# Optimization experiments

Measured on AMD Instinct MI355X. Metric: run time of the kernel, lower is better.

Reference implementation:

```python
import jax, jax.numpy as jnp
import numpy as np
from functools import partial

F_DIM, DETER, STOCH, HEADS = 1024, 256, 1024, 8
HD = F_DIM // HEADS  # 128
LN_EPS = 1e-5


def _layer_norm(x, g, b):
    m = jnp.mean(x, axis=-1, keepdims=True)
    v = jnp.var(x, axis=-1, keepdims=True)
    return (x - m) * jax.lax.rsqrt(v + LN_EPS) * g + b


def _forward(emb_vision, emb_text, emb_proprio, noise, h0, s0,
             proj_vision_w, proj_vision_b, proj_text_w, proj_text_b,
             proj_proprio_w, proj_proprio_b,
             attn_in_w, attn_in_b, attn_out_w, attn_out_b, importance,
             fuse_w1, fuse_b1, fuse_w2, fuse_b2, ln_g, ln_b,
             gru_w_ih, gru_w_hh, gru_b_ih, gru_b_hh,
             prior_w, prior_b, post_w, post_b):
    B, T = emb_vision.shape[:2]
    N = B * T
    # --- multimodal fusion, vectorized over all (B,T) steps ---
    pv = emb_vision @ proj_vision_w.T + proj_vision_b      # (B,T,F)
    pt = emb_text @ proj_text_w.T + proj_text_b
    pp = emb_proprio @ proj_proprio_w.T + proj_proprio_b
    stacked = jnp.stack([pv, pt, pp], axis=2).reshape(N, 3, F_DIM)  # (N,3,F)
    # self-attention over the 3 modality tokens (nn.MultiheadAttention)
    qkv = stacked @ attn_in_w.T + attn_in_b                 # (N,3,3F)
    q, k, v = jnp.split(qkv, 3, axis=-1)
    q = q.reshape(N, 3, HEADS, HD)
    k = k.reshape(N, 3, HEADS, HD)
    v = v.reshape(N, 3, HEADS, HD)
    scores = jnp.einsum('nqhd,nkhd->nhqk', q, k) / jnp.sqrt(jnp.float32(HD))
    attn = jax.nn.softmax(scores, axis=-1)
    att = jnp.einsum('nhqk,nkhd->nqhd', attn, v).reshape(N, 3, F_DIM)
    att = att @ attn_out_w.T + attn_out_b
    imp = jax.nn.softmax(importance)
    weighted = att * imp[None, :, None]
    concat = weighted.reshape(N, 3 * F_DIM)
    fused = jax.nn.relu(concat @ fuse_w1.T + fuse_b1) @ fuse_w2.T + fuse_b2
    fused = _layer_norm(fused, ln_g, ln_b).reshape(B, T, F_DIM)

    # --- sequential RSSM rollout ---
    def step(carry, xt):
        h, s = carry
        f_t, n_t = xt
        x = jnp.concatenate([s, f_t], axis=-1)              # (B, 2048)
        gi = x @ gru_w_ih.T + gru_b_ih                      # (B, 3*DETER)
        gh = h @ gru_w_hh.T + gru_b_hh
        ir, iz, inn = jnp.split(gi, 3, axis=-1)
        hr, hz, hn = jnp.split(gh, 3, axis=-1)
        r = jax.nn.sigmoid(ir + hr)
        z = jax.nn.sigmoid(iz + hz)
        n = jnp.tanh(inn + r * hn)
        h_new = (1.0 - z) * n + z * h
        prior = h_new @ prior_w.T + prior_b                 # (B, STOCH)
        post = jnp.concatenate([h_new, f_t], -1) @ post_w.T + post_b
        s_new = post + n_t                                  # reparameterized sample (unit std)
        out = jnp.concatenate([h_new, s_new, prior, post], axis=-1)
        return (h_new, s_new), out

    fused_T = jnp.swapaxes(fused, 0, 1)                     # (T,B,F)
    noise_T = jnp.swapaxes(noise, 0, 1)
    _, outs = jax.lax.scan(step, (h0, s0), (fused_T, noise_T))
    return jnp.swapaxes(outs, 0, 1)                         # (B,T,256+1024+1024+1024)


def setup_inputs() -> dict:
    key = jax.random.key(0)
    ks = iter(jax.random.split(key, 40))
    B, T = 64, 128

    def w(shape):
        fan_in = shape[-1]
        return jax.random.normal(next(ks), shape, jnp.float32) / np.sqrt(fan_in)

    d = {
        'emb_vision': jax.random.normal(next(ks), (B, T, 512), jnp.float32),
        'emb_text': jax.random.normal(next(ks), (B, T, 512), jnp.float32),
        'emb_proprio': jax.random.normal(next(ks), (B, T, 256), jnp.float32),
        'noise': jax.random.normal(next(ks), (B, T, STOCH), jnp.float32),
        'h0': jnp.zeros((B, DETER), jnp.float32),
        's0': jnp.zeros((B, STOCH), jnp.float32),
        'proj_vision_w': w((F_DIM, 512)), 'proj_vision_b': jnp.zeros((F_DIM,), jnp.float32),
        'proj_text_w': w((F_DIM, 512)), 'proj_text_b': jnp.zeros((F_DIM,), jnp.float32),
        'proj_proprio_w': w((F_DIM, 256)), 'proj_proprio_b': jnp.zeros((F_DIM,), jnp.float32),
        'attn_in_w': w((3 * F_DIM, F_DIM)), 'attn_in_b': jnp.zeros((3 * F_DIM,), jnp.float32),
        'attn_out_w': w((F_DIM, F_DIM)), 'attn_out_b': jnp.zeros((F_DIM,), jnp.float32),
        'importance': jnp.ones((3,), jnp.float32),
        'fuse_w1': w((F_DIM, 3 * F_DIM)), 'fuse_b1': jnp.zeros((F_DIM,), jnp.float32),
        'fuse_w2': w((F_DIM, F_DIM)), 'fuse_b2': jnp.zeros((F_DIM,), jnp.float32),
        'ln_g': jnp.ones((F_DIM,), jnp.float32), 'ln_b': jnp.zeros((F_DIM,), jnp.float32),
        'gru_w_ih': w((3 * DETER, F_DIM + STOCH)), 'gru_w_hh': w((3 * DETER, DETER)),
        'gru_b_ih': jnp.zeros((3 * DETER,), jnp.float32), 'gru_b_hh': jnp.zeros((3 * DETER,), jnp.float32),
        'prior_w': w((STOCH, DETER)), 'prior_b': jnp.zeros((STOCH,), jnp.float32),
        'post_w': w((STOCH, DETER + F_DIM)), 'post_b': jnp.zeros((STOCH,), jnp.float32),
    }
    return d


def reference(emb_vision, emb_text, emb_proprio, noise, h0, s0,
              proj_vision_w, proj_vision_b, proj_text_w, proj_text_b,
              proj_proprio_w, proj_proprio_b,
              attn_in_w, attn_in_b, attn_out_w, attn_out_b, importance,
              fuse_w1, fuse_b1, fuse_w2, fuse_b2, ln_g, ln_b,
              gru_w_ih, gru_w_hh, gru_b_ih, gru_b_hh,
              prior_w, prior_b, post_w, post_b):
    return _forward(emb_vision, emb_text, emb_proprio, noise, h0, s0,
                    proj_vision_w, proj_vision_b, proj_text_w, proj_text_b,
                    proj_proprio_w, proj_proprio_b,
                    attn_in_w, attn_in_b, attn_out_w, attn_out_b, importance,
                    fuse_w1, fuse_b1, fuse_w2, fuse_b2, ln_g, ln_b,
                    gru_w_ih, gru_w_hh, gru_b_ih, gru_b_hh,
                    prior_w, prior_b, post_w, post_b)
```

## Files before the change

kernel.cpp:

```cpp
#include <hip/hip_runtime.h>
#include <cstdint>
#include <cstddef>

#define F4(p)  (*(reinterpret_cast<float4*>(p)))
#define CF4(p) (*(reinterpret_cast<const float4*>(p)))

typedef __attribute__((ext_vector_type(8))) short short8;
typedef __attribute__((ext_vector_type(4))) float f32x4;
typedef __attribute__((ext_vector_type(4))) int i32x4;

__device__ __forceinline__ float bf2f(unsigned short h) {
  return __uint_as_float(((unsigned int)h) << 16);
}
__device__ __forceinline__ unsigned short f2bf(float x) {
  unsigned int u = __float_as_uint(x);
  return (unsigned short)((u + 0x7FFFu + ((u >> 16) & 1u)) >> 16);
}

#if __has_builtin(__builtin_amdgcn_global_load_lds)
#define USE_GLL 1
#else
#define USE_GLL 0
#endif
#if __has_builtin(__builtin_amdgcn_sched_barrier)
#define SCHED_BARRIER() __builtin_amdgcn_sched_barrier(0)
#else
#define SCHED_BARRIER()
#endif

__device__ __forceinline__ void stage16(unsigned short* lds_lane,
                                        unsigned short* lds_wavebase,
                                        const unsigned short* g) {
#if USE_GLL
  __builtin_amdgcn_global_load_lds(
      (const __attribute__((address_space(1))) unsigned int*)g,
      (__attribute__((address_space(3))) unsigned int*)lds_wavebase, 16, 0, 0);
#else
  *(short8*)lds_lane = *(const short8*)g;
#endif
}

__device__ __forceinline__ i32x4 coh_load16(const void* p) {
  i32x4 r;
  asm volatile("global_load_dwordx4 %0, %1, off sc0"
               : "=v"(r) : "v"(p) : "memory");
  return r;
}
__device__ __forceinline__ void coh_store16(void* p, i32x4 v) {
  asm volatile("global_store_dwordx4 %0, %1, off sc0"
               :: "v"(p), "v"(v) : "memory");
}

__device__ __forceinline__ float fsigmoid(float x) {
  return 1.0f / (1.0f + __expf(-x));
}
__device__ __forceinline__ float ftanh(float x) {
  float ax = fabsf(x);
  float e = __expf(2.0f * ax);
  float t = 1.0f - 2.0f / (e + 1.0f);
  return copysignf(t, x);
}

__global__ __launch_bounds__(256) void gemm_bf(
    const unsigned short* __restrict__ A, int lda,
    const unsigned short* __restrict__ A2, int lda2, int kSplit,
    const unsigned short* __restrict__ B, int ldb,
    const unsigned short* __restrict__ B2, int ldb2, int nSplit,
    void* __restrict__ Cv, int ldc, int K,
    const float* __restrict__ bias,
    const float* __restrict__ src, int ldsrc, int src_c0,
    const float* __restrict__ scale_ptr, int relu, int obf16, int qperm)
{
  __shared__ unsigned short As[128 * 64];
  __shared__ unsigned short Bs[128 * 64];
  const int tid = threadIdx.x;
  const int wv = tid >> 6, ln = tid & 63;
  const int wm = wv >> 1, wn = wv & 1;
  const size_t gm0 = (size_t)blockIdx.y * 128;
  const size_t gn0 = (size_t)blockIdx.x * 128;

  f32x4 acc[4][4];
  #pragma unroll
  for (int i = 0; i < 4; ++i)
    #pragma unroll
    for (int j = 0; j < 4; ++j) acc[i][j] = (f32x4){0.f, 0.f, 0.f, 0.f};

  for (int kk = 0; kk < K; kk += 64) {
    const unsigned short* Ause = A; int lduse = lda; int kkA = kk;
    if (A2 != nullptr && kk >= kSplit) { Ause = A2; lduse = lda2; kkA = kk - kSplit; }
    #pragma unroll
    for (int j = 0; j < 4; ++j) {
      int idx = j * 256 + tid;
      int r = idx >> 3, u = idx & 7;
      int ksw = (u ^ (r & 7)) << 3;
      const unsigned short* ga = Ause + (gm0 + r) * lduse + kkA + ksw;
      stage16(&As[idx * 8], &As[(idx & ~63) * 8], ga);
      size_t nr = gn0 + r;
      const unsigned short* gb = (nr < (size_t)nSplit)
          ? B + nr * ldb + kk + ksw
          : B2 + (nr - nSplit) * ldb2 + kk + ksw;
      stage16(&Bs[idx * 8], &Bs[(idx & ~63) * 8], gb);
    }
    __syncthreads();
    #pragma unroll
    for (int ks = 0; ks < 2; ++ks) {
      short8 af[4], bfv[4];
      #pragma unroll
      for (int mi = 0; mi < 4; ++mi) {
        int r = wm * 64 + mi * 16 + (ln & 15);
        int u = (ks * 4 + (ln >> 4)) ^ (r & 7);
        af[mi] = *(const short8*)&As[(r * 8 + u) * 8];
      }
      #pragma unroll
      for (int nj = 0; nj < 4; ++nj) {
        int r = wn * 64 + nj * 16 + (ln & 15);
        int u = (ks * 4 + (ln >> 4)) ^ (r & 7);
        bfv[nj] = *(const short8*)&Bs[(r * 8 + u) * 8];
      }
      #pragma unroll
      for (int mi = 0; mi < 4; ++mi)
        #pragma unroll
        for (int nj = 0; nj < 4; ++nj)
          acc[mi][nj] = __builtin_amdgcn_mfma_f32_16x16x32_bf16(
              af[mi], bfv[nj], acc[mi][nj], 0, 0, 0);
    }
    __syncthreads();
  }

  float sc = scale_ptr ? *scale_ptr : 1.0f;
  #pragma unroll
  for (int nj = 0; nj < 4; ++nj) {
    int gc = (int)gn0 + wn * 64 + nj * 16 + (ln & 15);
    float bv = bias ? bias[gc] : 0.f;
    #pragma unroll
    for (int mi = 0; mi < 4; ++mi) {
      #pragma unroll
      for (int qq = 0; qq < 4; ++qq) {
        int gr = (int)gm0 + wm * 64 + mi * 16 + ((ln >> 4) << 2) + qq;
        float v = acc[mi][nj][qq] * sc + bv;
        if (src && gc >= src_c0) v += src[(size_t)gr * ldsrc + (gc - src_c0)];
        if (relu) v = fmaxf(v, 0.f);
        if (qperm) {
          int t = gr & 127, bq = gr >> 7;
          int g = gc >> 8, d = gc & 255;
          int ddq = d >> 5, doff = d & 31;
          int wq = bq >> 4;
          int lq = (bq & 15) + ((doff >> 3) << 4);
          size_t qi = (((((size_t)t * 8 + ddq) * 3 + g) * 4 + wq) * 64 + lq) * 8
                      + (doff & 7);
          ((float*)Cv)[qi] = v;
        } else if (obf16) {
          ((unsigned short*)Cv)[(size_t)gr * ldc + gc] = f2bf(v);
        } else {
          ((float*)Cv)[(size_t)gr * ldc + gc] = v;
        }
      }
    }
  }
}

__global__ __launch_bounds__(256) void cvt_bf(
    const float* __restrict__ in, unsigned short* __restrict__ outp, int n4)
{
  int i = blockIdx.x * 256 + threadIdx.x;
  if (i < n4) {
    float4 v = CF4(in + (size_t)i * 4);
    ushort4 o;
    o.x = f2bf(v.x); o.y = f2bf(v.y); o.z = f2bf(v.z); o.w = f2bf(v.w);
    *(ushort4*)(outp + (size_t)i * 4) = o;
  }
}

__global__ __launch_bounds__(256) void transpose_bf(
    const float* __restrict__ in, int ldin, unsigned short* __restrict__ outp, int R)
{
  __shared__ float tile[32][33];
  int c0 = blockIdx.x * 32, r0 = blockIdx.y * 32;
  int tx = threadIdx.x & 31, ty = threadIdx.x >> 5;
  #pragma unroll
  for (int i = ty; i < 32; i += 8)
    tile[i][tx] = in[(size_t)(r0 + i) * ldin + c0 + tx];
  __syncthreads();
  #pragma unroll
  for (int i = ty; i < 32; i += 8)
    outp[(size_t)(c0 + i) * R + r0 + tx] = f2bf(tile[tx][i]);
}

__global__ __launch_bounds__(64) void matvec3(
    const float* __restrict__ A,
    const float* __restrict__ x0, const float* __restrict__ x1,
    const float* __restrict__ x2, const float* __restrict__ aib,
    float* __restrict__ outp)
{
  int i = blockIdx.x, t = threadIdx.x;
  const float* Ar = A + (size_t)i * 1024;
  float s0 = 0.f, s1 = 0.f, s2 = 0.f;
  for (int k = t * 4; k < 1024; k += 256) {
    float4 a = CF4(Ar + k);
    float4 v0 = CF4(x0 + k), v1 = CF4(x1 + k), v2 = CF4(x2 + k);
    s0 += a.x*v0.x + a.y*v0.y + a.z*v0.z + a.w*v0.w;
    s1 += a.x*v1.x + a.y*v1.y + a.z*v1.z + a.w*v1.w;
    s2 += a.x*v2.x + a.y*v2.y + a.z*v2.z + a.w*v2.w;
  }
  #pragma unroll
  for (int m = 32; m > 0; m >>= 1) {
    s0 += __shfl_xor(s0, m); s1 += __shfl_xor(s1, m); s2 += __shfl_xor(s2, m);
  }
  if (t == 0) {
    float b = aib[i];
    outp[i] = s0 + b; outp[3072 + i] = s1 + b; outp[6144 + i] = s2 + b;
  }
}

__global__ __launch_bounds__(64) void matvec_nt(
    const float* __restrict__ A, int lda,
    const float* __restrict__ x, const float* __restrict__ badd,
    float* __restrict__ outp, int K)
{
  int i = blockIdx.x, t = threadIdx.x;
  const float* Ar = A + (size_t)i * lda;
  float s = 0.f;
  for (int k = t * 4; k < K; k += 256) {
    float4 a = CF4(Ar + k);
    float4 xx = CF4(x + k);
    s += a.x*xx.x + a.y*xx.y + a.z*xx.z + a.w*xx.w;
  }
  #pragma unroll
  for (int m = 32; m > 0; m >>= 1) s += __shfl_xor(s, m);
  if (t == 0) outp[i] = s + (badd ? badd[i] : 0.f);
}

__global__ __launch_bounds__(256) void imp_rep_k(
    const float* __restrict__ importance, const float* __restrict__ aob,
    float* __restrict__ imp, float* __restrict__ rep)
{
  __shared__ float si[3];
  if (threadIdx.x == 0) {
    float a = importance[0], b = importance[1], c = importance[2];
    float mx = fmaxf(a, fmaxf(b, c));
    float ea = expf(a - mx), eb = expf(b - mx), ec = expf(c - mx);
    float inv = 1.f / (ea + eb + ec);
    si[0] = ea * inv; si[1] = eb * inv; si[2] = ec * inv;
    imp[0] = si[0]; imp[1] = si[1]; imp[2] = si[2];
  }
  __syncthreads();
  for (int idx = threadIdx.x; idx < 3072; idx += 256)
    rep[idx] = si[idx >> 10] * aob[idx & 1023];
}

__global__ __launch_bounds__(256) void bias_prep(
    const float* __restrict__ gbih, const float* __restrict__ gbhh,
    const float* __restrict__ prb, float* __restrict__ cb768,
    float* __restrict__ cb2048)
{
  int i = blockIdx.x * 256 + threadIdx.x;
  if (i < 768) cb768[i] = gbih[i] + (i < 512 ? gbhh[i] : 0.f);
  if (i < 2048) cb2048[i] = (i < 1024) ? prb[i] : 0.f;
}

__global__ __launch_bounds__(256) void attn3(
    const unsigned short* __restrict__ qkv, unsigned short* __restrict__ att)
{
  const int n = blockIdx.x;
  const unsigned short* row = qkv + (size_t)n * 9216;
  __shared__ float qk[6144];
  __shared__ float sc[72];
  __shared__ float pw[72];
  const int t = threadIdx.x;
  for (int idx = t; idx < 768; idx += 256) {
    int m = idx >> 7;
    int off = (idx & 127) << 3;
    const unsigned short* srcp = (m < 3) ? (row + m * 3072 + off)
                                         : (row + (m - 3) * 3072 + 1024 + off);
    short8 v = *(const short8*)srcp;
    float* dst = &qk[m * 1024 + off];
    #pragma unroll
    for (int j = 0; j < 8; ++j) dst[j] = bf2f(((const unsigned short*)&v)[j]);
  }
  __syncthreads();
  if (t < 72) {
    int h = t / 9, i = (t % 9) / 3, j = t % 3;
    const float* qp = &qk[i * 1024 + h * 128];
    const float* kp = &qk[3072 + j * 1024 + h * 128];
    float s = 0.f;
    int rot = (t & 31) * 4;
    for (int d2 = 0; d2 < 128; ++d2) {
      int dx = (d2 + rot) & 127;
      s += qp[dx] * kp[dx];
    }
    sc[t] = s * 0.08838834764831845f;
  }
  __syncthreads();
  if (t < 24) {
    int base = t * 3;
    float a = sc[base], b = sc[base + 1], c = sc[base + 2];
    float mx = fmaxf(a, fmaxf(b, c));
    float ea = expf(a - mx), eb = expf(b - mx), ec = expf(c - mx);
    float inv = 1.f / (ea + eb + ec);
    pw[base] = ea * inv; pw[base + 1] = eb * inv; pw[base + 2] = ec * inv;
  }
  __syncthreads();
  unsigned short* outp = att + (size_t)n * 3072;
  #pragma unroll
  for (int rep = 0; rep < 3; ++rep) {
    int idx = (rep * 256 + t) << 2;
    int i = idx >> 10;
    int hd = idx & 1023;
    int h = hd >> 7;
    int pb = (h * 3 + i) * 3;
    float w0 = pw[pb], w1 = pw[pb + 1], w2 = pw[pb + 2];
    ushort4 v0 = *(const ushort4*)(row + 2048 + hd);
    ushort4 v1 = *(const ushort4*)(row + 3072 + 2048 + hd);
    ushort4 v2 = *(const ushort4*)(row + 6144 + 2048 + hd);
    ushort4 o;
    o.x = f2bf(w0 * bf2f(v0.x) + w1 * bf2f(v1.x) + w2 * bf2f(v2.x));
    o.y = f2bf(w0 * bf2f(v0.y) + w1 * bf2f(v1.y) + w2 * bf2f(v2.y));
    o.z = f2bf(w0 * bf2f(v0.z) + w1 * bf2f(v1.z) + w2 * bf2f(v2.z));
    o.w = f2bf(w0 * bf2f(v0.w) + w1 * bf2f(v1.w) + w2 * bf2f(v2.w));
    *(ushort4*)(outp + idx) = o;
  }
}

__global__ __launch_bounds__(256) void layernorm_bf(
    unsigned short* __restrict__ X, const float* __restrict__ g,
    const float* __restrict__ bta)
{
  int n = blockIdx.x, t = threadIdx.x;
  unsigned short* row = X + (size_t)n * 1024;
  ushort4 hv = *(ushort4*)(row + t * 4);
  float x0 = bf2f(hv.x), x1 = bf2f(hv.y), x2 = bf2f(hv.z), x3 = bf2f(hv.w);
  float s = x0 + x1 + x2 + x3;
  float ss = x0*x0 + x1*x1 + x2*x2 + x3*x3;
  #pragma unroll
  for (int m = 32; m > 0; m >>= 1) { s += __shfl_xor(s, m); ss += __shfl_xor(ss, m); }
  __shared__ float rs[4], rss[4];
  int w = t >> 6;
  if ((t & 63) == 0) { rs[w] = s; rss[w] = ss; }
  __syncthreads();
  s = rs[0] + rs[1] + rs[2] + rs[3];
  ss = rss[0] + rss[1] + rss[2] + rss[3];
  float mean = s * (1.0f / 1024.0f);
  float var = ss * (1.0f / 1024.0f) - mean * mean;
  float inv = 1.0f / sqrtf(var + 1e-5f);
  float4 gg = CF4(g + t * 4);
  float4 bb = CF4(bta + t * 4);
  ushort4 o;
  o.x = f2bf((x0 - mean) * inv * gg.x + bb.x);
  o.y = f2bf((x1 - mean) * inv * gg.y + bb.y);
  o.z = f2bf((x2 - mean) * inv * gg.z + bb.z);
  o.w = f2bf((x3 - mean) * inv * gg.w + bb.w);
  *(ushort4*)(row + t * 4) = o;
}

__global__ __launch_bounds__(256) void build_R_bf(
    const float* __restrict__ Fpb, const float* __restrict__ noise,
    const float* __restrict__ s0, unsigned short* __restrict__ R)
{
  size_t idx = (size_t)blockIdx.x * 256 + threadIdx.x;
  int n = (int)(idx >> 8);
  int k4 = (int)(idx & 255) << 2;
  float4 v;
  if ((n & 127) == 0) {
    v = CF4(s0 + (size_t)(n >> 7) * 1024 + k4);
  } else {
    float4 f = CF4(Fpb + (size_t)(n - 1) * 1024 + k4);
    float4 z = CF4(noise + (size_t)(n - 1) * 1024 + k4);
    v.x = f.x + z.x; v.y = f.y + z.y; v.z = f.z + z.z; v.w = f.w + z.w;
  }
  ushort4 o;
  o.x = f2bf(v.x); o.y = f2bf(v.y); o.z = f2bf(v.z); o.w = f2bf(v.w);
  *(ushort4*)(R + (size_t)n * 1024 + k4) = o;
}

__global__ __launch_bounds__(256) void s_out_k(
    float* __restrict__ outp, const float* __restrict__ noise)
{
  size_t idx = (size_t)blockIdx.x * 256 + threadIdx.x;
  int n = (int)(idx >> 8);
  int j4 = (int)(idx & 255) << 2;
  float4 p = CF4(outp + (size_t)n * 3328 + 2304 + j4);
  float4 z = CF4(noise + (size_t)n * 1024 + j4);
  float4 o; o.x = p.x + z.x; o.y = p.y + z.y; o.z = p.z + z.z; o.w = p.w + z.w;
  F4(outp + (size_t)n * 3328 + 256 + j4) = o;
}

__global__ __launch_bounds__(256) void wr_prep(
    const unsigned short* __restrict__ M1bf, const unsigned short* __restrict__ Whhbf,
    unsigned short* __restrict__ Wr)
{
  int idx = blockIdx.x * 256 + threadIdx.x;
  int j = idx & 7, l = (idx >> 3) & 63, kt = (idx >> 9) & 7;
  int rest = idx >> 12;
  int r = rest % 12, dd = rest / 12;
  int g = r >> 1, dhalf = r & 1;
  int d = dd * 32 + dhalf * 16 + (l & 15);
  int srow = (g % 3) * 256 + d;
  int k = kt * 32 + ((l >> 4) << 3) + j;
  const unsigned short* srcp = (g < 3) ? M1bf : Whhbf;
  Wr[idx] = srcp[(size_t)srow * 256 + k];
}

__global__ __launch_bounds__(256) void h0_prep(
    const float* __restrict__ h0, unsigned short* __restrict__ hist)
{
  int idx = blockIdx.x * 256 + threadIdx.x;
  int j = idx & 7, l = (idx >> 3) & 63, kt = (idx >> 9) & 7, w = idx >> 12;
  int b = 16 * w + (l & 15);
  int k = kt * 32 + ((l >> 4) << 3) + j;
  hist[idx] = f2bf(h0[(size_t)b * 256 + k]);
}

#define LOADQ(tt) do { \
  _Pragma("unroll") \
  for (int g = 0; g < 3; ++g) { \
    const float* qp = Qr + (((((size_t)(tt) * 8 + dd) * 3 + g) * 4 + w) * 64 + l) * 8; \
    float4 qa = CF4(qp); float4 qb = CF4(qp + 4); \
    qv[g][0] = qa.x; qv[g][1] = qa.y; qv[g][2] = qa.z; qv[g][3] = qa.w; \
    qv[g][4] = qb.x; qv[g][5] = qb.y; qv[g][6] = qb.z; qv[g][7] = qb.w; \
  } } while (0)

__global__ __launch_bounds__(256, 1) void rssm_recur6(
    const unsigned short* __restrict__ Wr, const float* __restrict__ Qr,
    const float* __restrict__ bhh_n, unsigned short* __restrict__ hist,
    unsigned short* __restrict__ Hrow, float* __restrict__ outp,
    unsigned int* __restrict__ counters)
{
  const int tid = threadIdx.x;
  __shared__ int s_role;
  if (tid == 0) {
    unsigned int xcc;
    asm volatile("s_getreg_b32 %0, hwreg(HW_REG_XCC_ID)" : "=s"(xcc));
    int role = -1;
    if ((xcc & 7u) == 0u) {
      unsigned int r = __hip_atomic_fetch_add(&counters[8], 1u, __ATOMIC_RELAXED,
                                              __HIP_MEMORY_SCOPE_AGENT);
      if (r < 8u) role = (int)r;
    }
    s_role = role;
  }
  __syncthreads();
  const int dd = s_role;
  if (dd < 0) return;

  const int w = tid >> 6, l = tid & 63;
  __shared__ float G[12][16][68];
  __shared__ unsigned short hL[16384];

  short8 Bf[3][8];
  {
    const unsigned short* wb = Wr + ((size_t)(dd * 12 + w * 3) * 8) * 512 + l * 8;
    #pragma unroll
    for (int ri = 0; ri < 3; ++ri)
      #pragma unroll
      for (int kt = 0; kt < 8; ++kt)
        Bf[ri][kt] = *(const short8*)(wb + (size_t)(ri * 8 + kt) * 512);
  }
  float bhn[8];
  #pragma unroll
  for (int j = 0; j < 8; ++j) bhn[j] = bhh_n[dd * 32 + ((l >> 4) << 3) + j];

  const int bg = w * 16 + (l & 15);
  const int dhalf = l >> 5;
  const int d16b = ((l >> 4) & 1) << 3;
  float qv[3][8];
  LOADQ(0);

  unsigned int target = 0;
  #pragma unroll 1
  for (int t = 0; t < 128; ++t) {
    const unsigned short* hsrc = hist + (size_t)(t & 1) * 16384;
    i32x4 sv[8];
    #pragma unroll
    for (int j = 0; j < 8; ++j)
      sv[j] = coh_load16(hsrc + (size_t)(j * 256 + tid) * 8);
    asm volatile("s_waitcnt vmcnt(0)" ::: "memory");
    SCHED_BARRIER();
    #pragma unroll
    for (int j = 0; j < 8; ++j)
      *(i32x4*)&hL[(size_t)(j * 256 + tid) * 8] = sv[j];
    __syncthreads();

    f32x4 acc[4][3];
    #pragma unroll
    for (int bt = 0; bt < 4; ++bt)
      #pragma unroll
      for (int ri = 0; ri < 3; ++ri) acc[bt][ri] = (f32x4){0.f, 0.f, 0.f, 0.f};
    #pragma unroll
    for (int kt = 0; kt < 8; ++kt)
      #pragma unroll
      for (int bt = 0; bt < 4; ++bt) {
        short8 a = *(const short8*)&hL[((bt * 8 + kt) * 64 + l) * 8];
        acc[bt][0] = __builtin_amdgcn_mfma_f32_16x16x32_bf16(a, Bf[0][kt], acc[bt][0], 0, 0, 0);
        acc[bt][1] = __builtin_amdgcn_mfma_f32_16x16x32_bf16(a, Bf[1][kt], acc[bt][1], 0, 0, 0);
        acc[bt][2] = __builtin_amdgcn_mfma_f32_16x16x32_bf16(a, Bf[2][kt], acc[bt][2], 0, 0, 0);
      }
    short8 ha = *(const short8*)&hL[((w * 8 + dd) * 64 + l) * 8];

    #pragma unroll
    for (int bt = 0; bt < 4; ++bt)
      #pragma unroll
      for (int ri = 0; ri < 3; ++ri)
        *(f32x4*)&G[w * 3 + ri][l & 15][bt * 16 + ((l >> 4) << 2)] = acc[bt][ri];
    __syncthreads();

    const float m1s = (t == 0) ? 0.f : 1.f;
    unsigned short hn8[8];
    float hf8[8];
    #pragma unroll
    for (int j = 0; j < 8; ++j) {
      int d16 = d16b + j;
      float m1r = G[0 + dhalf][d16][bg];
      float m1z = G[2 + dhalf][d16][bg];
      float m1n = G[4 + dhalf][d16][bg];
      float ghr = G[6 + dhalf][d16][bg];
      float ghz = G[8 + dhalf][d16][bg];
      float ghn = G[10 + dhalf][d16][bg] + bhn[j];
      float gir = fmaf(m1r, m1s, qv[0][j]);
      float giz = fmaf(m1z, m1s, qv[1][j]);
      float gin = fmaf(m1n, m1s, qv[2][j]);
      float r = fsigmoid(gir + ghr);
      float z = fsigmoid(giz + ghz);
      float nn = ftanh(gin + r * ghn);
      float hold = bf2f(((const unsigned short*)&ha)[j]);
      float hn = (1.f - z) * nn + z * hold;
      unsigned short hbv = f2bf(hn);
      hn8[j] = hbv;
      hf8[j] = bf2f(hbv);
    }

    union { short8 s; i32x4 i; } hu;
    hu.s = *(const short8*)hn8;
    coh_store16(hist + (size_t)((t + 1) & 1) * 16384
                + (size_t)((w * 8 + dd) * 64 + l) * 8, hu.i);

    if (t < 127) {
      asm volatile("s_waitcnt vmcnt(0)" ::: "memory");
      __syncthreads();
      target += 8;
      if (tid == 0)
        __hip_atomic_fetch_add(&counters[0], 1u, __ATOMIC_RELAXED,
                               __HIP_MEMORY_SCOPE_AGENT);
      LOADQ(t + 1);
      *(short8*)(Hrow + (size_t)(bg * 128 + t) * 256 + dd * 32 + ((l >> 4) << 3)) =
          *(const short8*)hn8;
      float* op = outp + (size_t)(bg * 128 + t) * 3328 + dd * 32 + ((l >> 4) << 3);
      float4 o0; o0.x = hf8[0]; o0.y = hf8[1]; o0.z = hf8[2]; o0.w = hf8[3];
      float4 o1; o1.x = hf8[4]; o1.y = hf8[5]; o1.z = hf8[6]; o1.w = hf8[7];
      F4(op) = o0; F4(op + 4) = o1;
      if (tid == 0) {
        while (__hip_atomic_load(&counters[0], __ATOMIC_RELAXED,
                                 __HIP_MEMORY_SCOPE_AGENT) < target) {}
      }
      __syncthreads();
    } else {
      *(short8*)(Hrow + (size_t)(bg * 128 + t) * 256 + dd * 32 + ((l >> 4) << 3)) =
          *(const short8*)hn8;
      float* op = outp + (size_t)(bg * 128 + t) * 3328 + dd * 32 + ((l >> 4) << 3);
      float4 o0; o0.x = hf8[0]; o0.y = hf8[1]; o0.z = hf8[2]; o0.w = hf8[3];
      float4 o1; o1.x = hf8[4]; o1.y = hf8[5]; o1.z = hf8[6]; o1.w = hf8[7];
      F4(op) = o0; F4(op + 4) = o1;
    }
  }
}

static inline void g_bf(const unsigned short* A, int lda,
                        const unsigned short* B, int ldb,
                        void* C, int ldc, int M, int N, int K,
                        const float* bias, const float* src, int ldsrc,
                        const float* scale, int relu, int obf16, hipStream_t s,
                        const unsigned short* A2 = nullptr, int lda2 = 0,
                        int kSplit = 1 << 30,
                        const unsigned short* B2 = nullptr, int ldb2 = 0,
                        int nSplit = 1 << 30,
                        int src_c0 = 0, int qperm = 0)
{
  dim3 grid(N / 128, M / 128);
  gemm_bf<<<grid, 256, 0, s>>>(A, lda, A2, lda2, kSplit, B, ldb, B2, ldb2, nSplit,
                               C, ldc, K, bias, src, ldsrc, src_c0, scale, relu,
                               obf16, qperm);
}

extern "C" void kernel_launch(void* const* d_in, const int* in_sizes, int n_in,
                              void* d_out, int out_size, void* d_ws, size_t ws_size,
                              hipStream_t stream)
{
  (void)in_sizes; (void)n_in; (void)out_size;

  const float* emb_v = (const float*)d_in[0];
  const float* emb_t = (const float*)d_in[1];
  const float* emb_p = (const float*)d_in[2];
  const float* noise = (const float*)d_in[3];
  const float* h0    = (const float*)d_in[4];
  const float* s0    = (const float*)d_in[5];
  const float* pvw   = (const float*)d_in[6];
  const float* pvb   = (const float*)d_in[7];
  const float* ptw   = (const float*)d_in[8];
  const float* ptb   = (const float*)d_in[9];
  const float* ppw   = (const float*)d_in[10];
  const float* ppb   = (const float*)d_in[11];
  const float* aiw   = (const float*)d_in[12];
  const float* aib   = (const float*)d_in[13];
  const float* aow   = (const float*)d_in[14];
  const float* aob   = (const float*)d_in[15];
  const float* importance = (const float*)d_in[16];
  const float* fw1   = (const float*)d_in[17];
  const float* fb1   = (const float*)d_in[18];
  const float* fw2   = (const float*)d_in[19];
  const float* fb2   = (const float*)d_in[20];
  const float* ln_g  = (const float*)d_in[21];
  const float* ln_b  = (const float*)d_in[22];
  const float* gwih  = (const float*)d_in[23];
  const float* gwhh  = (const float*)d_in[24];
  const float* gbih  = (const float*)d_in[25];
  const float* gbhh  = (const float*)d_in[26];
  const float* prw   = (const float*)d_in[27];
  const float* prb   = (const float*)d_in[28];
  const float* pow_  = (const float*)d_in[29];
  const float* pob   = (const float*)d_in[30];

  float* out = (float*)d_out;
  char* W = (char*)d_ws;

  size_t off = 0;
  auto alloc = [&](size_t bytes) { off = (off + 63) & ~63ull; size_t o = off; off += bytes; return o; };
  const size_t o_cnt    = alloc(256);
  const size_t o_imp    = alloc(16);
  const size_t o_rep    = alloc(3072 * 4);
  const size_t o_bqkv   = alloc(9216 * 4);
  const size_t o_bf1    = alloc(1024 * 4);
  const size_t o_cb768  = alloc(768 * 4);
  const size_t o_cb2048 = alloc(2048 * 4);
  const size_t o_gwihb  = alloc(768ull * 2048 * 2);
  const size_t o_whhb   = alloc(768ull * 256 * 2);
  const size_t o_m1b    = alloc(768ull * 256 * 2);
  const size_t o_prwb   = alloc(1024ull * 256 * 2);
  const size_t o_powb   = alloc(1024ull * 1280 * 2);
  const size_t o_wr     = alloc(393216ull * 2);
  const size_t o_hist   = alloc(2ull * 16384 * 2);
  const size_t o_hrow   = alloc(8192ull * 256 * 2);
  const size_t o_fusedb = alloc(8192ull * 1024 * 2);
  const size_t o_fpb    = alloc(8192ull * 1024 * 4);
  const size_t o_rbf    = alloc(8192ull * 1024 * 2);
  const size_t o_embvb  = alloc(8192ull * 512 * 2);
  const size_t o_embtb  = alloc(8192ull * 512 * 2);
  const size_t o_embpb  = alloc(8192ull * 256 * 2);
  const size_t o_wqv    = alloc(3072ull * 512 * 2);
  const size_t o_wqt    = alloc(3072ull * 512 * 2);
  const size_t o_wqp    = alloc(3072ull * 256 * 2);
  const size_t o_wf1    = alloc(1024ull * 3072 * 2);
  const size_t o_fw2b   = alloc(1024ull * 1024 * 2);
  const size_t o_fused1 = alloc(8192ull * 1024 * 2);
  const size_t o_sub    = (off + 63) & ~63ull;

  const size_t so_aiwb = 0;
  const size_t so_fw1b = so_aiwb + 3072ull * 1024 * 2;
  const size_t so_pTv  = so_fw1b + 1024ull * 3072 * 2;
  const size_t so_pTt  = so_pTv + 512ull * 1024 * 2;
  const size_t so_pTp  = so_pTt + 512ull * 1024 * 2;
  const size_t so_aoT  = so_pTp + 256ull * 1024 * 2;
  const size_t so_WphT = so_aoT + 1024ull * 1024 * 2;
  const size_t prep_bytes = so_WphT + 256ull * 1024 * 2;
  const size_t q_bytes = 8192ull * 768 * 4;

  int NC = 512;
  for (int cand : {8192, 4096, 2048, 1024}) {
    size_t sub = prep_bytes > q_bytes ? prep_bytes : q_bytes;
    size_t cb = (size_t)cand * 9216 * 2 + (size_t)cand * 3072 * 2;
    if (cb > sub) sub = cb;
    if (o_sub + sub <= ws_size) { NC = cand; break; }
  }
  const size_t o_qkvc = o_sub;
  const size_t o_attc = o_sub + (size_t)NC * 9216 * 2;
  const size_t o_qr   = o_sub;

  auto FP = [&](size_t o) { return (float*)(W + o); };
  auto UP = [&](size_t o) { return (unsigned short*)(W + o); };

  hipMemsetAsync(W + o_cnt, 0, 256, stream);
  imp_rep_k<<<1, 256, 0, stream>>>(importance, aob, FP(o_imp), FP(o_rep));
  bias_prep<<<8, 256, 0, stream>>>(gbih, gbhh, prb, FP(o_cb768), FP(o_cb2048));

  auto cvt = [&](const float* in, unsigned short* op, size_t n) {
    int n4 = (int)(n / 4);
    cvt_bf<<<(n4 + 255) / 256, 256, 0, stream>>>(in, op, n4);
  };
  cvt(aiw,  UP(o_sub + so_aiwb), 3072ull * 1024);
  cvt(fw1,  UP(o_sub + so_fw1b), 1024ull * 3072);
  cvt(fw2,  UP(o_fw2b), 1024ull * 1024);
  cvt(gwih, UP(o_gwihb), 768ull * 2048);
  cvt(gwhh, UP(o_whhb), 768ull * 256);
  cvt(prw,  UP(o_prwb), 1024ull * 256);
  cvt(pow_, UP(o_powb), 1024ull * 1280);
  cvt(emb_v, UP(o_embvb), 8192ull * 512);
  cvt(emb_t, UP(o_embtb), 8192ull * 512);
  cvt(emb_p, UP(o_embpb), 8192ull * 256);

  transpose_bf<<<dim3(16, 32), 256, 0, stream>>>(pvw, 512, UP(o_sub + so_pTv), 1024);
  transpose_bf<<<dim3(16, 32), 256, 0, stream>>>(ptw, 512, UP(o_sub + so_pTt), 1024);
  transpose_bf<<<dim3(8, 32), 256, 0, stream>>>(ppw, 256, UP(o_sub + so_pTp), 1024);
  transpose_bf<<<dim3(32, 32), 256, 0, stream>>>(aow, 1024, UP(o_sub + so_aoT), 1024);
  transpose_bf<<<dim3(8, 32), 256, 0, stream>>>(pow_, 1280, UP(o_sub + so_WphT), 1024);

  matvec3<<<3072, 64, 0, stream>>>(aiw, pvb, ptb, ppb, aib, FP(o_bqkv));
  matvec_nt<<<1024, 64, 0, stream>>>(fw1, 3072, FP(o_rep), fb1, FP(o_bf1), 3072);

  g_bf(UP(o_sub + so_aiwb), 1024, UP(o_sub + so_pTv), 1024, UP(o_wqv), 512,
       3072, 512, 1024, nullptr, nullptr, 0, nullptr, 0, 1, stream);
  g_bf(UP(o_sub + so_aiwb), 1024, UP(o_sub + so_pTt), 1024, UP(o_wqt), 512,
       3072, 512, 1024, nullptr, nullptr, 0, nullptr, 0, 1, stream);
  g_bf(UP(o_sub + so_aiwb), 1024, UP(o_sub + so_pTp), 1024, UP(o_wqp), 256,
       3072, 256, 1024, nullptr, nullptr, 0, nullptr, 0, 1, stream);
  for (int m = 0; m < 3; ++m)
    g_bf(UP(o_sub + so_fw1b) + m * 1024, 3072, UP(o_sub + so_aoT), 1024,
         UP(o_wf1) + m * 1024, 3072, 1024, 1024, 1024,
         nullptr, nullptr, 0, FP(o_imp) + m, 0, 1, stream);
  g_bf(UP(o_gwihb), 2048, UP(o_sub + so_WphT), 1024, UP(o_m1b), 256,
       768, 256, 1024, nullptr, nullptr, 0, nullptr, 0, 1, stream);

  wr_prep<<<1536, 256, 0, stream>>>(UP(o_m1b), UP(o_whhb), UP(o_wr));
  h0_prep<<<64, 256, 0, stream>>>(h0, UP(o_hist));

  const int nchunk = 8192 / NC;
  for (int c = 0; c < nchunk; ++c) {
    g_bf(UP(o_embvb) + (size_t)c * NC * 512, 512, UP(o_wqv), 512,
         UP(o_qkvc) + 0, 9216, NC, 3072, 512, FP(o_bqkv) + 0,
         nullptr, 0, nullptr, 0, 1, stream);
    g_bf(UP(o_embtb) + (size_t)c * NC * 512, 512, UP(o_wqt), 512,
         UP(o_qkvc) + 3072, 9216, NC, 3072, 512, FP(o_bqkv) + 3072,
         nullptr, 0, nullptr, 0, 1, stream);
    g_bf(UP(o_embpb) + (size_t)c * NC * 256, 256, UP(o_wqp), 256,
         UP(o_qkvc) + 6144, 9216, NC, 3072, 256, FP(o_bqkv) + 6144,
         nullptr, 0, nullptr, 0, 1, stream);
    attn3<<<NC, 256, 0, stream>>>(UP(o_qkvc), UP(o_attc));
    g_bf(UP(o_attc), 3072, UP(o_wf1), 3072,
         UP(o_fused1) + (size_t)c * NC * 1024, 1024, NC, 1024, 3072,
         FP(o_bf1), nullptr, 0, nullptr, 1 , 1, stream);
  }

  g_bf(UP(o_fused1), 1024, UP(o_fw2b), 1024, UP(o_fusedb), 1024,
       8192, 1024, 1024, fb2, nullptr, 0, nullptr, 0, 1, stream);
  layernorm_bf<<<8192, 256, 0, stream>>>(UP(o_fusedb), ln_g, ln_b);

  g_bf(UP(o_fusedb), 1024, UP(o_powb) + 256, 1280, FP(o_fpb), 1024,
       8192, 1024, 1024, pob, nullptr, 0, nullptr, 0, 0, stream);
  build_R_bf<<<8192, 256, 0, stream>>>(FP(o_fpb), noise, s0, UP(o_rbf));
  g_bf(UP(o_rbf), 1024, UP(o_gwihb), 2048, FP(o_qr), 768,
       8192, 768, 2048, FP(o_cb768), nullptr, 0, nullptr, 0, 0, stream,
       UP(o_fusedb), 1024, 1024, nullptr, 0, 1 << 30, 0, 1 );

  rssm_recur6<<<256, 256, 0, stream>>>(UP(o_wr), FP(o_qr), gbhh + 512, UP(o_hist),
                                       UP(o_hrow), out, (unsigned int*)(W + o_cnt));

  g_bf(UP(o_hrow), 256, UP(o_prwb), 256, out + 1280, 3328,
       8192, 2048, 256, FP(o_cb2048), FP(o_fpb), 1024, nullptr, 0, 0, stream,
       nullptr, 0, 1 << 30, UP(o_powb), 1280, 1024, 1024 , 0);
  s_out_k<<<8192, 256, 0, stream>>>(out, noise);
}
```

Before: 1.359 ms.

## Use per-block flags in recurrence, fuse weight conversions, remap GEMM tiles per XCD

Measured after the change: 1.255 ms. 7.7% less time.

```diff
diff --git a/kernel.cpp b/kernel.cpp
--- a/kernel.cpp
+++ b/kernel.cpp
@@ -51,13 +51,18 @@
                :: "v"(p), "v"(v) : "memory");
 }
 
+__device__ __forceinline__ float frcp(float x) {
+  float r;
+  asm("v_rcp_f32 %0, %1" : "=v"(r) : "v"(x));
+  return r;
+}
 __device__ __forceinline__ float fsigmoid(float x) {
-  return 1.0f / (1.0f + __expf(-x));
+  return frcp(1.0f + __expf(-x));
 }
 __device__ __forceinline__ float ftanh(float x) {
   float ax = fabsf(x);
   float e = __expf(2.0f * ax);
-  float t = 1.0f - 2.0f / (e + 1.0f);
+  float t = 1.0f - 2.0f * frcp(e + 1.0f);
   return copysignf(t, x);
 }
 
@@ -76,8 +81,14 @@
   const int tid = threadIdx.x;
   const int wv = tid >> 6, ln = tid & 63;
   const int wm = wv >> 1, wn = wv & 1;
-  const size_t gm0 = (size_t)blockIdx.y * 128;
-  const size_t gn0 = (size_t)blockIdx.x * 128;
+
+  int nwg = (int)(gridDim.x * gridDim.y);
+  int orig = (int)(blockIdx.y * gridDim.x + blockIdx.x);
+  int q8 = nwg >> 3, r8 = nwg & 7;
+  int xcd = orig & 7, ii = orig >> 3;
+  int wg = (xcd < r8 ? xcd * (q8 + 1) : r8 * (q8 + 1) + (xcd - r8) * q8) + ii;
+  const size_t gm0 = (size_t)(wg / (int)gridDim.x) * 128;
+  const size_t gn0 = (size_t)(wg % (int)gridDim.x) * 128;
 
   f32x4 acc[4][4];
   #pragma unroll
@@ -159,15 +170,26 @@
   }
 }
 
-__global__ __launch_bounds__(256) void cvt_bf(
-    const float* __restrict__ in, unsigned short* __restrict__ outp, int n4)
-{
-  int i = blockIdx.x * 256 + threadIdx.x;
-  if (i < n4) {
-    float4 v = CF4(in + (size_t)i * 4);
+struct CvtArgs {
+  const float* src[10];
+  unsigned short* dst[10];
+  int bend[10];
+  int n4[10];
+};
+
+__global__ __launch_bounds__(256) void cvt_all(CvtArgs a)
+{
+  int b = blockIdx.x;
+  int s = 0;
+  #pragma unroll
+  for (int k = 0; k < 10; ++k) s += (b >= a.bend[k]);
+  int bstart = (s == 0) ? 0 : a.bend[s - 1];
+  int i = (b - bstart) * 256 + threadIdx.x;
+  if (i < a.n4[s]) {
+    float4 v = CF4(a.src[s] + (size_t)i * 4);
     ushort4 o;
     o.x = f2bf(v.x); o.y = f2bf(v.y); o.z = f2bf(v.z); o.w = f2bf(v.w);
-    *(ushort4*)(outp + (size_t)i * 4) = o;
+    *(ushort4*)(a.dst[s] + (size_t)i * 4) = o;
   }
 }
 
@@ -419,7 +441,21 @@
     qv[g][4] = qb.x; qv[g][5] = qb.y; qv[g][6] = qb.z; qv[g][7] = qb.w; \
   } } while (0)
 
-__global__ __launch_bounds__(256, 1) void rssm_recur6(
+#define STAGE_H(buf_idx) do { \
+  const unsigned short* hsrc = hist + (size_t)(buf_idx) * 16384; \
+  i32x4 sv[8]; \
+  _Pragma("unroll") \
+  for (int j = 0; j < 8; ++j) \
+    sv[j] = coh_load16(hsrc + (size_t)(j * 256 + tid) * 8); \
+  asm volatile("s_waitcnt vmcnt(0)" ::: "memory"); \
+  SCHED_BARRIER(); \
+  _Pragma("unroll") \
+  for (int j = 0; j < 8; ++j) \
+    *(i32x4*)&hL[(size_t)(j * 256 + tid) * 8] = sv[j]; \
+  __syncthreads(); \
+} while (0)
+
+__global__ __launch_bounds__(256, 1) void rssm_recur7(
     const unsigned short* __restrict__ Wr, const float* __restrict__ Qr,
     const float* __restrict__ bhh_n, unsigned short* __restrict__ hist,
     unsigned short* __restrict__ Hrow, float* __restrict__ outp,
@@ -464,22 +500,10 @@
   const int d16b = ((l >> 4) & 1) << 3;
   float qv[3][8];
   LOADQ(0);
-
-  unsigned int target = 0;
+  STAGE_H(0);
+
   #pragma unroll 1
   for (int t = 0; t < 128; ++t) {
-    const unsigned short* hsrc = hist + (size_t)(t & 1) * 16384;
-    i32x4 sv[8];
-    #pragma unroll
-    for (int j = 0; j < 8; ++j)
-      sv[j] = coh_load16(hsrc + (size_t)(j * 256 + tid) * 8);
-    asm volatile("s_waitcnt vmcnt(0)" ::: "memory");
-    SCHED_BARRIER();
-    #pragma unroll
-    for (int j = 0; j < 8; ++j)
-      *(i32x4*)&hL[(size_t)(j * 256 + tid) * 8] = sv[j];
-    __syncthreads();
-
     f32x4 acc[4][3];
     #pragma unroll
     for (int bt = 0; bt < 4; ++bt)
@@ -536,22 +560,24 @@
     if (t < 127) {
       asm volatile("s_waitcnt vmcnt(0)" ::: "memory");
       __syncthreads();
-      target += 8;
       if (tid == 0)
-        __hip_atomic_fetch_add(&counters[0], 1u, __ATOMIC_RELAXED,
-                               __HIP_MEMORY_SCOPE_AGENT);
-      LOADQ(t + 1);
+        __hip_atomic_store(&counters[16 + dd * 16], (unsigned int)(t + 1),
+                           __ATOMIC_RELAXED, __HIP_MEMORY_SCOPE_AGENT);
       *(short8*)(Hrow + (size_t)(bg * 128 + t) * 256 + dd * 32 + ((l >> 4) << 3)) =
           *(const short8*)hn8;
       float* op = outp + (size_t)(bg * 128 + t) * 3328 + dd * 32 + ((l >> 4) << 3);
       float4 o0; o0.x = hf8[0]; o0.y = hf8[1]; o0.z = hf8[2]; o0.w = hf8[3];
       float4 o1; o1.x = hf8[4]; o1.y = hf8[5]; o1.z = hf8[6]; o1.w = hf8[7];
       F4(op) = o0; F4(op + 4) = o1;
-      if (tid == 0) {
-        while (__hip_atomic_load(&counters[0], __ATOMIC_RELAXED,
-                                 __HIP_MEMORY_SCOPE_AGENT) < target) {}
+      LOADQ(t + 1);
+      const unsigned int tgt = (unsigned int)(t + 1);
+      while (true) {
+        unsigned int v = __hip_atomic_load(&counters[16 + (l & 7) * 16],
+                                           __ATOMIC_RELAXED,
+                                           __HIP_MEMORY_SCOPE_AGENT);
+        if (__all((int)(v >= tgt))) break;
       }
-      __syncthreads();
+      STAGE_H((t + 1) & 1);
     } else {
       *(short8*)(Hrow + (size_t)(bg * 128 + t) * 256 + dd * 32 + ((l >> 4) << 3)) =
           *(const short8*)hn8;
@@ -623,7 +649,7 @@
 
   size_t off = 0;
   auto alloc = [&](size_t bytes) { off = (off + 63) & ~63ull; size_t o = off; off += bytes; return o; };
-  const size_t o_cnt    = alloc(256);
+  const size_t o_cnt    = alloc(2048);
   const size_t o_imp    = alloc(16);
   const size_t o_rep    = alloc(3072 * 4);
   const size_t o_bqkv   = alloc(9216 * 4);
@@ -676,24 +702,31 @@
   auto FP = [&](size_t o) { return (float*)(W + o); };
   auto UP = [&](size_t o) { return (unsigned short*)(W + o); };
 
-  hipMemsetAsync(W + o_cnt, 0, 256, stream);
+  hipMemsetAsync(W + o_cnt, 0, 2048, stream);
   imp_rep_k<<<1, 256, 0, stream>>>(importance, aob, FP(o_imp), FP(o_rep));
   bias_prep<<<8, 256, 0, stream>>>(gbih, gbhh, prb, FP(o_cb768), FP(o_cb2048));
 
-  auto cvt = [&](const float* in, unsigned short* op, size_t n) {
-    int n4 = (int)(n / 4);
-    cvt_bf<<<(n4 + 255) / 256, 256, 0, stream>>>(in, op, n4);
-  };
-  cvt(aiw,  UP(o_sub + so_aiwb), 3072ull * 1024);
-  cvt(fw1,  UP(o_sub + so_fw1b), 1024ull * 3072);
-  cvt(fw2,  UP(o_fw2b), 1024ull * 1024);
-  cvt(gwih, UP(o_gwihb), 768ull * 2048);
-  cvt(gwhh, UP(o_whhb), 768ull * 256);
-  cvt(prw,  UP(o_prwb), 1024ull * 256);
-  cvt(pow_, UP(o_powb), 1024ull * 1280);
-  cvt(emb_v, UP(o_embvb), 8192ull * 512);
-  cvt(emb_t, UP(o_embtb), 8192ull * 512);
-  cvt(emb_p, UP(o_embpb), 8192ull * 256);
+  {
+    CvtArgs a;
+    const float* srcs[10] = {aiw, fw1, fw2, gwih, gwhh, prw, pow_,
+                             emb_v, emb_t, emb_p};
+    unsigned short* dsts[10] = {
+        UP(o_sub + so_aiwb), UP(o_sub + so_fw1b), UP(o_fw2b), UP(o_gwihb),
+        UP(o_whhb), UP(o_prwb), UP(o_powb),
+        UP(o_embvb), UP(o_embtb), UP(o_embpb)};
+    const size_t n4s[10] = {3072ull*1024/4, 1024ull*3072/4, 1024ull*1024/4,
+                            768ull*2048/4, 768ull*256/4, 1024ull*256/4,
+                            1024ull*1280/4,
+                            8192ull*512/4, 8192ull*512/4, 8192ull*256/4};
+    int cum = 0;
+    for (int k = 0; k < 10; ++k) {
+      a.src[k] = srcs[k]; a.dst[k] = dsts[k];
+      a.n4[k] = (int)n4s[k];
+      cum += (int)((n4s[k] + 255) / 256);
+      a.bend[k] = cum;
+    }
+    cvt_all<<<cum, 256, 0, stream>>>(a);
+  }
 
   transpose_bf<<<dim3(16, 32), 256, 0, stream>>>(pvw, 512, UP(o_sub + so_pTv), 1024);
   transpose_bf<<<dim3(16, 32), 256, 0, stream>>>(ptw, 512, UP(o_sub + so_pTt), 1024);
@@ -748,7 +781,7 @@
        8192, 768, 2048, FP(o_cb768), nullptr, 0, nullptr, 0, 0, stream,
        UP(o_fusedb), 1024, 1024, nullptr, 0, 1 << 30, 0, 1 );
 
-  rssm_recur6<<<256, 256, 0, stream>>>(UP(o_wr), FP(o_qr), gbhh + 512, UP(o_hist),
+  rssm_recur7<<<256, 256, 0, stream>>>(UP(o_wr), FP(o_qr), gbhh + 512, UP(o_hist),
                                        UP(o_hrow), out, (unsigned int*)(W + o_cnt));
 
   g_bf(UP(o_hrow), 256, UP(o_prwb), 256, out + 1280, 3328,
```
